# Optimization experiments

Measured on AMD Instinct MI355X. Metric: run time of the kernel, lower is better.

Reference implementation:

```python
import jax, jax.numpy as jnp
import numpy as np

D = 256; H = 8; HD = D // H; DEPTH = 4
NGRIDS = 512; TILE = 256; IN_CHANS = 1536
MAX_SEQ = (131072 // TILE) ** 2  # 262144
_SEGS = [int(v) for v in 2.0 ** np.linspace(np.log2(1024.0), np.log2(float(MAX_SEQ)), 5)]  # [1024,4096,16384,65536,262144]
_RATIOS = [1, 2, 4, 8, 16]
LN_EPS = 1e-5


def build_pos_embed(dim, gs):
    # MAE-style 2d sincos pos embed with a leading zero row for the cls token.
    def emb1d(d, pos):
        omega = 1.0 / 10000 ** (np.arange(d // 2, dtype=np.float64) / (d / 2.0))
        out = np.einsum('m,d->md', pos.reshape(-1).astype(np.float64), omega)
        return np.concatenate([np.sin(out), np.cos(out)], axis=1)
    g = np.arange(gs, dtype=np.float64)
    gw, gh = np.meshgrid(g, g)  # meshgrid(grid_w, grid_h) as in MAE
    emb = np.concatenate([emb1d(dim // 2, gw), emb1d(dim // 2, gh)], axis=1)  # (gs*gs, dim)
    return np.concatenate([np.zeros((1, dim)), emb], axis=0).astype(np.float32)


def _ln(x, w, b):
    mu = x.mean(-1, keepdims=True)
    var = ((x - mu) ** 2).mean(-1, keepdims=True)
    return (x - mu) * jax.lax.rsqrt(var + LN_EPS) * w + b


def _dilated_attn(x, wqkv, bqkv, wo, bo):
    # LongNet dilated attention: for each (segment_len w, dilation r) branch,
    # attend within segments over a per-head strided subsample (offset = head % r),
    # then combine branches weighted by softmax log-sum-exp.
    B, L, _ = x.shape
    q, k, v = jnp.split(x @ wqkv + bqkv, 3, axis=-1)
    q = q.reshape(B, L, H, HD); k = k.reshape(B, L, H, HD); v = v.reshape(B, L, H, HD)
    scale = 1.0 / np.sqrt(HD)
    outs, lses = [], []
    for w_seg, r in zip(_SEGS, _RATIOS):
        we = min(w_seg, L); we = max((we // r) * r, r)   # effective segment length
        Lp = -(-L // we) * we; pad = Lp - L; n = Lp // we; m = we // r
        idx = (jnp.arange(H) % r)[:, None] + r * jnp.arange(m)[None, :]  # (H, m) per-head strided idx
        def seg(t):
            tp = jnp.pad(t, ((0, 0), (0, pad), (0, 0), (0, 0)))
            tp = tp.reshape(B, n, we, H, HD).transpose(0, 1, 3, 2, 4)  # (B,n,H,we,HD)
            return jnp.take_along_axis(tp, idx[None, None, :, :, None], axis=3)  # (B,n,H,m,HD)
        qs, ks, vs = seg(q), seg(k), seg(v)
        valid = (jnp.arange(Lp) < L).reshape(n, we)[:, idx]  # (n,H,m) key validity (padding mask)
        s = jnp.einsum('bnhqd,bnhkd->bnhqk', qs, ks) * scale
        s = jnp.where(valid[None, :, :, None, :], s, -jnp.inf)
        mx = jnp.maximum(jnp.max(s, axis=-1, keepdims=True), -1e30)
        p = jnp.exp(s - mx)
        den = jnp.sum(p, axis=-1, keepdims=True)
        o = jnp.einsum('bnhqk,bnhkd->bnhqd', p, vs) / jnp.maximum(den, 1e-30)
        lse = mx[..., 0] + jnp.log(jnp.maximum(den[..., 0], 1e-30))  # (B,n,H,m)
        hidx = jnp.arange(H)[:, None]
        of = jnp.zeros((B, n, H, we, HD), x.dtype).at[:, :, hidx, idx].set(o)
        lf = jnp.full((B, n, H, we), -jnp.inf, x.dtype).at[:, :, hidx, idx].set(lse)
        outs.append(of.transpose(0, 1, 3, 2, 4).reshape(B, Lp, H, HD)[:, :L])
        lses.append(lf.transpose(0, 1, 3, 2).reshape(B, Lp, H)[:, :L])
    lse_all = jnp.stack(lses)                         # (S,B,L,H)
    out_all = jnp.stack(outs)                         # (S,B,L,H,HD)
    wgt = jnp.exp(lse_all - jnp.max(lse_all, axis=0, keepdims=True))
    o = jnp.sum(wgt[..., None] * out_all, axis=0) / jnp.sum(wgt, axis=0)[..., None]
    return o.reshape(B, L, D) @ wo + bo


def _forward(x, coords, patch_w, patch_b, cls_token, pos_embed, ln1_w, ln1_b, wqkv, bqkv,
             wo, bo, ln2_w, ln2_b, w1, b1, w2, b2, encln_w, encln_b, norm_w, norm_b):
    B = x.shape[0]
    h = x @ patch_w + patch_b                                   # patch embed (Linear)
    g = jnp.floor(coords / TILE)
    pos = (g[..., 0] * NGRIDS + g[..., 1]).astype(jnp.int32) + 1  # coords_to_pos
    h = h + pos_embed[pos]                                      # irregular pos-embed gather
    cls = jnp.broadcast_to(cls_token + pos_embed[0], (B, 1, D))
    h = jnp.concatenate([cls, h], axis=1)                       # (B, 4096, D)

    def step(hc, p):
        l1w, l1b, qw, qb, ow, ob, l2w, l2b, f1w, f1b, f2w, f2b = p
        hc = hc + _dilated_attn(_ln(hc, l1w, l1b), qw, qb, ow, ob)
        f = jax.nn.gelu(_ln(hc, l2w, l2b) @ f1w + f1b, approximate=False) @ f2w + f2b
        return hc + f, None

    h, _ = jax.lax.scan(step, h, (ln1_w, ln1_b, wqkv, bqkv, wo, bo, ln2_w, ln2_b, w1, b1, w2, b2))
    h = _ln(h, encln_w, encln_b)          # encoder final LN (pre-LN stack)
    return _ln(h, norm_w, norm_b)[:, 0]   # global_pool=False: normed cls token, (B, D)


def setup_inputs() -> dict:
    key = jax.random.key(0)
    ks = jax.random.split(key, 8)
    B, N = 1, 4095
    s = 0.02
    rn = lambda k, shape: jax.random.normal(k, shape, jnp.float32) * s
    return dict(
        x=jax.random.normal(ks[0], (B, N, IN_CHANS), jnp.float32),
        coords=jax.random.randint(ks[1], (B, N, 2), 0, TILE * NGRIDS).astype(jnp.float32),
        patch_w=rn(ks[2], (IN_CHANS, D)), patch_b=jnp.zeros((D,), jnp.float32),
        cls_token=rn(ks[3], (1, 1, D)),
        pos_embed=jnp.asarray(build_pos_embed(D, NGRIDS)),
        ln1_w=jnp.ones((DEPTH, D), jnp.float32), ln1_b=jnp.zeros((DEPTH, D), jnp.float32),
        wqkv=rn(ks[4], (DEPTH, D, 3 * D)), bqkv=jnp.zeros((DEPTH, 3 * D), jnp.float32),
        wo=rn(ks[5], (DEPTH, D, D)), bo=jnp.zeros((DEPTH, D), jnp.float32),
        ln2_w=jnp.ones((DEPTH, D), jnp.float32), ln2_b=jnp.zeros((DEPTH, D), jnp.float32),
        w1=rn(ks[6], (DEPTH, D, 4 * D)), b1=jnp.zeros((DEPTH, 4 * D), jnp.float32),
        w2=rn(ks[7], (DEPTH, 4 * D, D)), b2=jnp.zeros((DEPTH, D), jnp.float32),
        encln_w=jnp.ones((D,), jnp.float32), encln_b=jnp.zeros((D,), jnp.float32),
        norm_w=jnp.ones((D,), jnp.float32), norm_b=jnp.zeros((D,), jnp.float32),
    )


def reference(x, coords, patch_w, patch_b, cls_token, pos_embed, ln1_w, ln1_b, wqkv, bqkv,
              wo, bo, ln2_w, ln2_b, w1, b1, w2, b2, encln_w, encln_b, norm_w, norm_b):
    return _forward(x, coords, patch_w, patch_b, cls_token, pos_embed, ln1_w, ln1_b, wqkv, bqkv,
                    wo, bo, ln2_w, ln2_b, w1, b1, w2, b2, encln_w, encln_b, norm_w, norm_b)
```

## Files before the change

kernel.cpp:

```cpp
#include <hip/hip_runtime.h>
#include <hip/hip_bf16.h>
#include <math.h>


typedef __attribute__((ext_vector_type(8))) short short8;
typedef __attribute__((ext_vector_type(4))) float f32x4;

__device__ __forceinline__ float wred_sum(float v) {
#pragma unroll
  for (int o = 32; o; o >>= 1) v += __shfl_xor(v, o);
  return v;
}

__device__ __forceinline__ unsigned short f2bf(float x) {
  unsigned u = __float_as_uint(x);
  u += 0x7FFF + ((u >> 16) & 1);
  return (unsigned short)(u >> 16);
}
__device__ __forceinline__ float bf2f(unsigned short s) {
  return __uint_as_float(((unsigned)s) << 16);
}

__global__ __launch_bounds__(256) void prep_kernel(
    const float* __restrict__ pw, const float* __restrict__ wqkv,
    const float* __restrict__ wo, const float* __restrict__ w1,
    const float* __restrict__ w2, unsigned short* __restrict__ wt,
    const float* __restrict__ x, unsigned short* __restrict__ xb) {
  __shared__ float T[32][33];
  if (blockIdx.x >= 3456) {
    const int i = (blockIdx.x - 3456) * 256 + threadIdx.x;
    const int row = i / 192, k8 = i % 192;
    const int k = k8 * 8;
    size_t dst = ((size_t)(row >> 4) * 48 + (k >> 5)) * 512 +
                 (size_t)(row & 15) * 32 + (k & 31);
    if (row >= 4095) {
      *(uint4*)(xb + dst) = make_uint4(0, 0, 0, 0);
      return;
    }
    const float4 a = *(const float4*)(x + (size_t)row * 1536 + k);
    const float4 b = *(const float4*)(x + (size_t)row * 1536 + k + 4);
    unsigned u0 = (unsigned)f2bf(a.x) | ((unsigned)f2bf(a.y) << 16);
    unsigned u1 = (unsigned)f2bf(a.z) | ((unsigned)f2bf(a.w) << 16);
    unsigned u2 = (unsigned)f2bf(b.x) | ((unsigned)f2bf(b.y) << 16);
    unsigned u3 = (unsigned)f2bf(b.z) | ((unsigned)f2bf(b.w) << 16);
    *(uint4*)(xb + dst) = make_uint4(u0, u1, u2, u3);
    return;
  }
  const int bid = blockIdx.x;
  const float* src;
  int Kd, Nd, lt;
  size_t doff;
  if (bid < 384) {
    src = pw; Kd = 1536; Nd = 256; doff = 0; lt = bid;
  } else if (bid < 1152) {
    int l = (bid - 384) / 192, r = (bid - 384) % 192;
    src = wqkv + (size_t)l * 196608; Kd = 256; Nd = 768;
    doff = 393216 + (size_t)l * 196608; lt = r;
  } else if (bid < 1408) {
    int l = (bid - 1152) / 64, r = (bid - 1152) % 64;
    src = wo + (size_t)l * 65536; Kd = 256; Nd = 256;
    doff = 1179648 + (size_t)l * 65536; lt = r;
  } else if (bid < 2432) {
    int l = (bid - 1408) / 256, r = (bid - 1408) % 256;
    src = w1 + (size_t)l * 262144; Kd = 256; Nd = 1024;
    doff = 1441792 + (size_t)l * 262144; lt = r;
  } else {
    int l = (bid - 2432) / 256, r = (bid - 2432) % 256;
    src = w2 + (size_t)l * 262144; Kd = 1024; Nd = 256;
    doff = 2490368 + (size_t)l * 262144; lt = r;
  }
  const int tilesK = Kd >> 5;
  const int tn = lt / tilesK, tk = lt % tilesK;
  const int k0 = tk * 32, n0 = tn * 32;
  const int t = threadIdx.x;
  const int rr = t >> 3, c4 = t & 7;
  float4 v = *(const float4*)(src + (size_t)(k0 + rr) * Nd + n0 + c4 * 4);
  T[rr][c4 * 4 + 0] = v.x;
  T[rr][c4 * 4 + 1] = v.y;
  T[rr][c4 * 4 + 2] = v.z;
  T[rr][c4 * 4 + 3] = v.w;
  __syncthreads();
  float o0 = T[c4 * 4 + 0][rr], o1 = T[c4 * 4 + 1][rr];
  float o2 = T[c4 * 4 + 2][rr], o3 = T[c4 * 4 + 3][rr];
  unsigned u0 = (unsigned)f2bf(o0) | ((unsigned)f2bf(o1) << 16);
  unsigned u1 = (unsigned)f2bf(o2) | ((unsigned)f2bf(o3) << 16);
  const int n = n0 + rr;
  size_t fo = doff + ((size_t)(n >> 4) * (Kd >> 5) + (k0 >> 5)) * 512 +
              (size_t)(n & 15) * 32 + c4 * 4;
  *(uint2*)(wt + fo) = make_uint2(u0, u1);
}

__global__ __launch_bounds__(256) void gemm_patch(
    const unsigned short* __restrict__ Af, const unsigned short* __restrict__ Bt,
    const float* __restrict__ bias, const float* __restrict__ coords,
    const float* __restrict__ cls, const float* __restrict__ pe,
    float* __restrict__ h) {
  const int lane = threadIdx.x & 63, w = threadIdx.x >> 6;
  const int g = lane >> 4, q = lane & 15;
  const int bm = blockIdx.x * 64, bn = blockIdx.y * 32;

  const unsigned short* ap =
      Af + ((size_t)((bm >> 4) + w) * 48) * 512 + q * 32 + 8 * g;
  const unsigned short* bp = Bt + q * 32 + 8 * g;

  f32x4 acc[2];
#pragma unroll
  for (int i = 0; i < 2; i++) acc[i] = (f32x4){0.f, 0.f, 0.f, 0.f};

#pragma unroll 4
  for (int ks = 0; ks < 48; ks++) {
    short8 af = *(const short8*)(ap + (size_t)ks * 512);
#pragma unroll
    for (int cf = 0; cf < 2; cf++) {
      short8 bf = *(const short8*)(bp +
          ((size_t)(((bn >> 4) + cf) * 48 + ks)) * 512);
      acc[cf] = __builtin_amdgcn_mfma_f32_16x16x32_bf16(af, bf, acc[cf], 0, 0, 0);
    }
  }

  const int orow0 = bm + 16 * w + 4 * g;
  int prow[4];
#pragma unroll
  for (int rg = 0; rg < 4; rg++) {
    int orow = orow0 + rg;
    orow = orow < 4095 ? orow : 4094;
    float c0 = coords[(size_t)orow * 2 + 0];
    float c1 = coords[(size_t)orow * 2 + 1];
    prow[rg] = (int)floorf(c0 * (1.f / 256.f)) * 512 +
               (int)floorf(c1 * (1.f / 256.f)) + 1;
  }
#pragma unroll
  for (int cf = 0; cf < 2; cf++) {
    const int col = bn + 16 * cf + q;
    const float bs = bias[col];
#pragma unroll
    for (int rg = 0; rg < 4; rg++) {
      int orow = orow0 + rg;
      if (orow < 4095) {
        float c = acc[cf][rg] + bs + pe[(size_t)prow[rg] * 256 + col];
        h[(size_t)(orow + 1) * 256 + col] = c;
      }
    }
  }
  if (blockIdx.x == 0 && blockIdx.y == 0 && threadIdx.x < 64) {
    float4 cv = *(const float4*)(cls + threadIdx.x * 4);
    float4 pv = *(const float4*)(pe + threadIdx.x * 4);
    *(float4*)(h + threadIdx.x * 4) =
        make_float4(cv.x + pv.x, cv.y + pv.y, cv.z + pv.z, cv.w + pv.w);
  }
}

__global__ __launch_bounds__(256) void ln_bf16_kernel(
    const float* __restrict__ x, const float* __restrict__ wg,
    const float* __restrict__ b, unsigned short* __restrict__ y) {
  const int row = blockIdx.x * 4 + (threadIdx.x >> 6);
  const int lane = threadIdx.x & 63;
  float4 v = *(const float4*)(x + (size_t)row * 256 + lane * 4);
  float s1 = wred_sum(v.x + v.y + v.z + v.w);
  float s2 = wred_sum(v.x * v.x + v.y * v.y + v.z * v.z + v.w * v.w);
  float mu = s1 * (1.f / 256.f);
  float inv = rsqrtf(s2 * (1.f / 256.f) - mu * mu + 1e-5f);
  float4 wv = *(const float4*)(wg + lane * 4);
  float4 bv = *(const float4*)(b + lane * 4);
  float o0 = (v.x - mu) * inv * wv.x + bv.x;
  float o1 = (v.y - mu) * inv * wv.y + bv.y;
  float o2 = (v.z - mu) * inv * wv.z + bv.z;
  float o3 = (v.w - mu) * inv * wv.w + bv.w;
  unsigned u0 = (unsigned)f2bf(o0) | ((unsigned)f2bf(o1) << 16);
  unsigned u1 = (unsigned)f2bf(o2) | ((unsigned)f2bf(o3) << 16);
  size_t addr = ((size_t)(row >> 4) * 8 + (lane >> 3)) * 512 +
                (size_t)(row & 15) * 32 + (lane & 7) * 4;
  *(uint2*)(y + addr) = make_uint2(u0, u1);
}

template <int EPI>
__global__ __launch_bounds__(256) void gemm_af(
    const unsigned short* __restrict__ Af, const unsigned short* __restrict__ Bt,
    const float* __restrict__ bias, unsigned short* __restrict__ Cv, int N) {
  const int lane = threadIdx.x & 63, w = threadIdx.x >> 6;
  const int g = lane >> 4, q = lane & 15;
  const int bm = blockIdx.x * 64, bn = blockIdx.y * 64;
  const unsigned short* ap =
      Af + ((size_t)((bm >> 4) + w) * 8) * 512 + q * 32 + 8 * g;
  const unsigned short* bp = Bt + q * 32 + 8 * g;

  f32x4 acc[4];
#pragma unroll
  for (int i = 0; i < 4; i++) acc[i] = (f32x4){0.f, 0.f, 0.f, 0.f};

#pragma unroll
  for (int ks = 0; ks < 8; ks++) {
    short8 af = *(const short8*)(ap + (size_t)ks * 512);
#pragma unroll
    for (int cf = 0; cf < 4; cf++) {
      short8 bf = *(const short8*)(bp +
          ((size_t)((bn >> 4) + cf) * 8 + ks) * 512);
      acc[cf] = __builtin_amdgcn_mfma_f32_16x16x32_bf16(af, bf, acc[cf], 0, 0, 0);
    }
  }

  const int orow0 = bm + 16 * w + 4 * g;
#pragma unroll
  for (int cf = 0; cf < 4; cf++) {
    const int col = bn + 16 * cf + q;
    const float bs = bias[col];
#pragma unroll
    for (int rg = 0; rg < 4; rg++) {
      float c = acc[cf][rg] + bs;
      const int orow = orow0 + rg;
      if (EPI == 1) {
        c = 0.5f * c * (1.f + erff(c * 0.70710678118654752f));
        const int cq = 16 * cf + q;
        size_t idx = ((size_t)(orow >> 4) * (N >> 5) + (bn >> 5) + (cq >> 5)) *
                         512 +
                     (size_t)(orow & 15) * 32 + (cq & 31);
        Cv[idx] = f2bf(c);
      } else {
        Cv[(size_t)orow * N + col] = f2bf(c);
      }
    }
  }
}

__global__ __launch_bounds__(256) void gemm_proj(
    const unsigned short* __restrict__ Af, const unsigned short* __restrict__ Bt,
    const float* __restrict__ bias, float* __restrict__ C) {
  const int lane = threadIdx.x & 63, w = threadIdx.x >> 6;
  const int g = lane >> 4, q = lane & 15;
  const int bm = blockIdx.x * 64, bn = blockIdx.y * 32;
  const unsigned short* ap =
      Af + ((size_t)((bm >> 4) + w) * 8) * 512 + q * 32 + 8 * g;
  const unsigned short* bp = Bt + q * 32 + 8 * g;

  f32x4 acc[2];
#pragma unroll
  for (int i = 0; i < 2; i++) acc[i] = (f32x4){0.f, 0.f, 0.f, 0.f};

#pragma unroll
  for (int ks = 0; ks < 8; ks++) {
    short8 af = *(const short8*)(ap + (size_t)ks * 512);
#pragma unroll
    for (int cf = 0; cf < 2; cf++) {
      short8 bf = *(const short8*)(bp +
          ((size_t)((bn >> 4) + cf) * 8 + ks) * 512);
      acc[cf] = __builtin_amdgcn_mfma_f32_16x16x32_bf16(af, bf, acc[cf], 0, 0, 0);
    }
  }

  const int orow0 = bm + 16 * w + 4 * g;
#pragma unroll
  for (int cf = 0; cf < 2; cf++) {
    const int col = bn + 16 * cf + q;
    const float bs = bias[col];
#pragma unroll
    for (int rg = 0; rg < 4; rg++)
      C[(size_t)(orow0 + rg) * 256 + col] += acc[cf][rg] + bs;
  }
}

__global__ __launch_bounds__(256) void gemm_mlp2(
    const unsigned short* __restrict__ Af, const unsigned short* __restrict__ Bt,
    const float* __restrict__ bias, float* __restrict__ C) {
  const int lane = threadIdx.x & 63, w = threadIdx.x >> 6;
  const int g = lane >> 4, q = lane & 15;
  const int bm = blockIdx.x * 64, bn = blockIdx.y * 32;
  const unsigned short* ap =
      Af + ((size_t)((bm >> 4) + w) * 32) * 512 + q * 32 + 8 * g;
  const unsigned short* bp = Bt + q * 32 + 8 * g;

  f32x4 acc[2];
#pragma unroll
  for (int i = 0; i < 2; i++) acc[i] = (f32x4){0.f, 0.f, 0.f, 0.f};

#pragma unroll 4
  for (int ks = 0; ks < 32; ks++) {
    short8 af = *(const short8*)(ap + (size_t)ks * 512);
#pragma unroll
    for (int cf = 0; cf < 2; cf++) {
      short8 bf = *(const short8*)(bp +
          ((size_t)((bn >> 4) + cf) * 32 + ks) * 512);
      acc[cf] = __builtin_amdgcn_mfma_f32_16x16x32_bf16(af, bf, acc[cf], 0, 0, 0);
    }
  }

  const int orow0 = bm + 16 * w + 4 * g;
#pragma unroll
  for (int cf = 0; cf < 2; cf++) {
    const int col = bn + 16 * cf + q;
    const float bs = bias[col];
#pragma unroll
    for (int rg = 0; rg < 4; rg++)
      C[(size_t)(orow0 + rg) * 256 + col] += acc[cf][rg] + bs;
  }
}

__device__ __forceinline__ void decode_gather(int bid, int& r, int& m,
                                              int& off, int& base, int& h,
                                              int& kt, int& ub) {
  const int c = bid & 7;
  const int j = bid >> 3;
  if (j < 64) {
    int u = c + 8 * (j >> 4);
    kt = j & 15;
    r = 1; m = 1024; base = (u >> 3) * 1024; h = u & 7; off = 0; ub = u * 32768;
  } else if (j < 96) {
    int jj = j - 64;
    int grp = c + 8 * (jj >> 4);
    h = grp >> 1;
    kt = (grp & 1) * 16 + (jj & 15);
    r = 2; m = 2048; base = 0; off = h & 1; ub = 1048576 + h * 65536;
  } else if (j < 112) {
    h = c; kt = j - 96;
    r = 4; m = 1024; base = 0; off = h & 3; ub = 1572864 + h * 32768;
  } else if (j < 120) {
    h = c; kt = j - 112;
    r = 8; m = 512; base = 0; off = h & 7; ub = 1835008 + h * 16384;
  } else {
    h = c; kt = j - 120;
    r = 16; m = 256; base = 0; off = h; ub = 1966080 + h * 8192;
  }
}

__global__ __launch_bounds__(256) void gather_kernel(
    const unsigned short* __restrict__ qkvb, unsigned short* __restrict__ kg,
    unsigned short* __restrict__ vt) {
  __shared__ unsigned short T[32][64];
  int r, m, off, base, h, kt, ub;
  decode_gather(blockIdx.x, r, m, off, base, h, kt, ub);
  const int t = threadIdx.x;
  {
    int key = t >> 2, c = t & 3;
    size_t row = base + off + (size_t)r * (kt * 64 + key);
    const unsigned short* src = qkvb + row * 768 + h * 32 + 8 * c;
    short8 kk = *(const short8*)(src + 256);
    int gk = kt * 64 + key;
    *(short8*)(kg + ub + (size_t)(gk >> 4) * 512 + (size_t)(gk & 15) * 32 +
               8 * c) = kk;
    short8 vv = *(const short8*)(src + 512);
#pragma unroll
    for (int i = 0; i < 8; i++) T[8 * c + i][key] = (unsigned short)vv[i];
  }
  __syncthreads();
  int dim = t >> 3, c8 = t & 7;
  int vk = kt * 64 + 8 * c8;
  *(short8*)(vt + ub + ((size_t)(vk >> 5) * 2 + (dim >> 4)) * 512 +
             (size_t)(dim & 15) * 32 + (vk & 31)) = *(const short8*)&T[dim][8 * c8];
}

__device__ __forceinline__ void decode_attn(int bid, int& slot, int& r, int& m,
                                            int& nt, int& koff, int& off,
                                            int& base, int& h, int& qt,
                                            int& ub) {
  const int c = bid & 7;
  const int j = bid >> 3;
  if (j < 64) {
    int u = c + 8 * (j >> 4);
    qt = j & 15;
    slot = 0; r = 1; m = 1024; nt = 16; koff = 0;
    base = (u >> 3) * 1024; h = u & 7; off = 0; ub = u * 32768;
  } else if (j < 128) {
    int jj = j - 64;
    int grp = c + 8 * (jj >> 5);
    h = grp >> 1;
    int half = grp & 1;
    qt = jj & 31;
    slot = 1 + half; r = 2; m = 2048; nt = 16; koff = half * 1024;
    base = 0; off = h & 1; ub = 1048576 + h * 65536;
  } else if (j < 144) {
    h = c; qt = j - 128;
    slot = 3; r = 4; m = 1024; nt = 16; koff = 0;
    base = 0; off = h & 3; ub = 1572864 + h * 32768;
  } else if (j < 152) {
    h = c; qt = j - 144;
    slot = 4; r = 8; m = 512; nt = 8; koff = 0;
    base = 0; off = h & 7; ub = 1835008 + h * 16384;
  } else {
    h = c; qt = j - 152;
    slot = 5; r = 16; m = 256; nt = 4; koff = 0;
    base = 0; off = h; ub = 1966080 + h * 8192;
  }
}

__global__ __launch_bounds__(256) void attn_mfma_kernel(
    const unsigned short* __restrict__ qkvb,
    const unsigned short* __restrict__ kg, const unsigned short* __restrict__ vt,
    unsigned short* __restrict__ oa, float* __restrict__ lse_all) {
  int slot, r, m, nt, koff, off, base, h, qt, ub;
  decode_attn(blockIdx.x, slot, r, m, nt, koff, off, base, h, qt, ub);

  const int lane = threadIdx.x & 63;
  const int wid = threadIdx.x >> 6;
  const int g = lane >> 4, q = lane & 15;
  const int q0 = qt * 64 + wid * 16;

  const size_t qrow = base + off + (size_t)r * (q0 + q);
  short8 qf = *(const short8*)(qkvb + qrow * 768 + h * 32 + 8 * g);

  const unsigned short* kp = kg + ub + q * 32 + 8 * g;
  const unsigned short* vp = vt + ub + q * 32 + 8 * g;
  const int kt0 = koff >> 4;
  const int vt0 = koff >> 5;

  f32x4 ot0 = {0.f, 0.f, 0.f, 0.f}, ot1 = {0.f, 0.f, 0.f, 0.f};
  float rl = 0.f;
  const float scale = 0.17677669529663687f;

  short8 kf[4];
#pragma unroll
  for (int a = 0; a < 4; a++)
    kf[a] = *(const short8*)(kp + (size_t)(kt0 + a) * 512);

  for (int kt = 0; kt < nt; ++kt) {
    const int k0 = kt * 64;
    const int v2 = vt0 + (k0 >> 5);
    short8 va0 = *(const short8*)(vp + (size_t)(v2 * 2 + 0) * 512);
    short8 vb0 = *(const short8*)(vp + (size_t)(v2 * 2 + 1) * 512);
    short8 va1 = *(const short8*)(vp + (size_t)((v2 + 1) * 2 + 0) * 512);
    short8 vb1 = *(const short8*)(vp + (size_t)((v2 + 1) * 2 + 1) * 512);

    f32x4 st[4];
#pragma unroll
    for (int a = 0; a < 4; a++) {
      f32x4 z = {0.f, 0.f, 0.f, 0.f};
      st[a] = __builtin_amdgcn_mfma_f32_16x16x32_bf16(kf[a], qf, z, 0, 0, 0);
    }
    if (kt + 1 < nt) {
#pragma unroll
      for (int a = 0; a < 4; a++)
        kf[a] = *(const short8*)(kp + (size_t)(kt0 + ((k0 + 64) >> 4) + a) * 512);
    }

    float p[4][4];
    float tl = 0.f;
#pragma unroll
    for (int a = 0; a < 4; a++)
#pragma unroll
      for (int rr = 0; rr < 4; rr++) {
        p[a][rr] = __expf(st[a][rr] * scale);
        tl += p[a][rr];
      }
    tl += __shfl_xor(tl, 16);
    tl += __shfl_xor(tl, 32);
    rl += tl;

    unsigned pk[4][2];
#pragma unroll
    for (int a = 0; a < 4; a++) {
      asm("v_cvt_pk_bf16_f32 %0, %1, %2"
          : "=v"(pk[a][0]) : "v"(p[a][0]), "v"(p[a][1]));
      asm("v_cvt_pk_bf16_f32 %0, %1, %2"
          : "=v"(pk[a][1]) : "v"(p[a][2]), "v"(p[a][3]));
    }

#pragma unroll
    for (int kk = 0; kk < 2; kk++) {
      union { unsigned w[4]; short8 v; } pb;
#pragma unroll
      for (int jj = 0; jj < 2; jj++) {
        int src = q + 16 * ((2 * g + jj) & 3);
#pragma unroll
        for (int d = 0; d < 2; d++) {
          unsigned lo = (unsigned)__shfl((int)pk[2 * kk + 0][d], src);
          unsigned hi = (unsigned)__shfl((int)pk[2 * kk + 1][d], src);
          pb.w[jj * 2 + d] = (g >> 1) ? hi : lo;
        }
      }
      if (kk == 0) {
        ot0 = __builtin_amdgcn_mfma_f32_16x16x32_bf16(va0, pb.v, ot0, 0, 0, 0);
        ot1 = __builtin_amdgcn_mfma_f32_16x16x32_bf16(vb0, pb.v, ot1, 0, 0, 0);
      } else {
        ot0 = __builtin_amdgcn_mfma_f32_16x16x32_bf16(va1, pb.v, ot0, 0, 0, 0);
        ot1 = __builtin_amdgcn_mfma_f32_16x16x32_bf16(vb1, pb.v, ot1, 0, 0, 0);
      }
    }
  }

  float inv = 1.f / rl;
  int pos = base + off + r * (q0 + q);
  size_t ob = (((size_t)(slot * 256 + (pos >> 4)) * 8 + h) * 16 + (pos & 15)) * 32;
  unsigned w0 = (unsigned)f2bf(ot0[0] * inv) | ((unsigned)f2bf(ot0[1] * inv) << 16);
  unsigned w1 = (unsigned)f2bf(ot0[2] * inv) | ((unsigned)f2bf(ot0[3] * inv) << 16);
  unsigned w2 = (unsigned)f2bf(ot1[0] * inv) | ((unsigned)f2bf(ot1[1] * inv) << 16);
  unsigned w3 = (unsigned)f2bf(ot1[2] * inv) | ((unsigned)f2bf(ot1[3] * inv) << 16);
  *(uint2*)(oa + ob + 4 * g) = make_uint2(w0, w1);
  *(uint2*)(oa + ob + 16 + 4 * g) = make_uint2(w2, w3);
  if (g == 0)
    lse_all[((size_t)slot * 4096 + pos) * 8 + h] = __logf(rl);
}

__global__ __launch_bounds__(256) void combine_kernel(
    const unsigned short* __restrict__ oa, const float* __restrict__ lse_all,
    unsigned short* __restrict__ attb) {
  const int pt = blockIdx.x >> 3, ph = blockIdx.x & 7;
  const int t = threadIdx.x;
  const int d0 = (t & 15) * 2;
  const int pl = t >> 4;
  const int pos = pt * 16 + pl;

  const int msk[6] = {0, 1, 1, 3, 7, 15};
  float l[6];
  bool cov[6];
#pragma unroll
  for (int s = 0; s < 6; s++) {
    cov[s] = ((pos ^ ph) & msk[s]) == 0;
    l[s] = cov[s] ? lse_all[((size_t)s * 4096 + pos) * 8 + ph] : -3.0e38f;
  }
  float mx = l[0];
#pragma unroll
  for (int s = 1; s < 6; s++) mx = fmaxf(mx, l[s]);
  float wsum = 0.f, o0 = 0.f, o1 = 0.f;
#pragma unroll
  for (int s = 0; s < 6; s++) {
    if (cov[s]) {
      float wg = __expf(l[s] - mx);
      wsum += wg;
      unsigned u = *(const unsigned*)(oa +
          (((size_t)(s * 256 + pt) * 8 + ph) * 16 + pl) * 32 + d0);
      o0 += wg * bf2f((unsigned short)(u & 0xFFFF));
      o1 += wg * bf2f((unsigned short)(u >> 16));
    }
  }
  float inv = 1.f / wsum;
  unsigned u = (unsigned)f2bf(o0 * inv) | ((unsigned)f2bf(o1 * inv) << 16);
  *(unsigned*)(attb + ((size_t)pt * 8 + ph) * 512 + pl * 32 + d0) = u;
}

__global__ __launch_bounds__(64) void final_kernel(
    const float* __restrict__ h, const float* __restrict__ ew,
    const float* __restrict__ eb, const float* __restrict__ nw,
    const float* __restrict__ nb, float* __restrict__ out) {
  const int lane = threadIdx.x;
  float4 v = *(const float4*)(h + lane * 4);
  float s1 = wred_sum(v.x + v.y + v.z + v.w);
  float s2 = wred_sum(v.x * v.x + v.y * v.y + v.z * v.z + v.w * v.w);
  float mu = s1 * (1.f / 256.f);
  float inv = rsqrtf(s2 * (1.f / 256.f) - mu * mu + 1e-5f);
  float4 wv = *(const float4*)(ew + lane * 4);
  float4 bv = *(const float4*)(eb + lane * 4);
  float4 tv;
  tv.x = (v.x - mu) * inv * wv.x + bv.x;
  tv.y = (v.y - mu) * inv * wv.y + bv.y;
  tv.z = (v.z - mu) * inv * wv.z + bv.z;
  tv.w = (v.w - mu) * inv * wv.w + bv.w;
  s1 = wred_sum(tv.x + tv.y + tv.z + tv.w);
  s2 = wred_sum(tv.x * tv.x + tv.y * tv.y + tv.z * tv.z + tv.w * tv.w);
  mu = s1 * (1.f / 256.f);
  inv = rsqrtf(s2 * (1.f / 256.f) - mu * mu + 1e-5f);
  float4 w2v = *(const float4*)(nw + lane * 4);
  float4 b2v = *(const float4*)(nb + lane * 4);
  float4 o;
  o.x = (tv.x - mu) * inv * w2v.x + b2v.x;
  o.y = (tv.y - mu) * inv * w2v.y + b2v.y;
  o.z = (tv.z - mu) * inv * w2v.z + b2v.z;
  o.w = (tv.w - mu) * inv * w2v.w + b2v.w;
  *(float4*)(out + lane * 4) = o;
}


extern "C" void kernel_launch(void* const* d_in, const int* in_sizes, int n_in,
                              void* d_out, int out_size, void* d_ws,
                              size_t ws_size, hipStream_t stream) {
  const float* x      = (const float*)d_in[0];
  const float* coords = (const float*)d_in[1];
  const float* pw     = (const float*)d_in[2];
  const float* pb     = (const float*)d_in[3];
  const float* cls    = (const float*)d_in[4];
  const float* pe     = (const float*)d_in[5];
  const float* ln1w   = (const float*)d_in[6];
  const float* ln1b   = (const float*)d_in[7];
  const float* wqkv   = (const float*)d_in[8];
  const float* bqkv   = (const float*)d_in[9];
  const float* wo     = (const float*)d_in[10];
  const float* bo     = (const float*)d_in[11];
  const float* ln2w   = (const float*)d_in[12];
  const float* ln2b   = (const float*)d_in[13];
  const float* w1     = (const float*)d_in[14];
  const float* b1     = (const float*)d_in[15];
  const float* w2     = (const float*)d_in[16];
  const float* b2     = (const float*)d_in[17];
  const float* encw   = (const float*)d_in[18];
  const float* encb   = (const float*)d_in[19];
  const float* nw     = (const float*)d_in[20];
  const float* nb     = (const float*)d_in[21];

  float* ws = (float*)d_ws;
  float* h              = ws;
  unsigned short* hnbf  = (unsigned short*)(ws + 1048576);
  unsigned short* qkvb  = (unsigned short*)(ws + 1572864);
  unsigned short* kg    = (unsigned short*)(ws + 3145728);
  unsigned short* vt    = (unsigned short*)(ws + 4161536);
  unsigned short* oa    = (unsigned short*)(ws + 5177344);
  float* lse            = ws + 8323072;
  unsigned short* attb  = (unsigned short*)(ws + 8519680);
  unsigned short* midb  = (unsigned short*)(ws + 9043968);
  unsigned short* xb    = (unsigned short*)(ws + 11141120);
  unsigned short* wt    = (unsigned short*)(ws + 14286848);

  prep_kernel<<<6528, 256, 0, stream>>>(pw, wqkv, wo, w1, w2, wt, x, xb);
  gemm_patch<<<dim3(64, 8), 256, 0, stream>>>(xb, wt, pb, coords, cls, pe, h);

  for (int l = 0; l < 4; l++) {
    ln_bf16_kernel<<<1024, 256, 0, stream>>>(h, ln1w + l * 256, ln1b + l * 256,
                                             hnbf);
    gemm_af<3><<<dim3(64, 12), 256, 0, stream>>>(
        hnbf, wt + 393216 + (size_t)l * 196608, bqkv + l * 768, qkvb, 768);
    gather_kernel<<<992, 256, 0, stream>>>(qkvb, kg, vt);
    attn_mfma_kernel<<<1248, 256, 0, stream>>>(qkvb, kg, vt, oa, lse);
    combine_kernel<<<2048, 256, 0, stream>>>(oa, lse, attb);
    gemm_proj<<<dim3(64, 8), 256, 0, stream>>>(
        attb, wt + 1179648 + (size_t)l * 65536, bo + l * 256, h);
    ln_bf16_kernel<<<1024, 256, 0, stream>>>(h, ln2w + l * 256, ln2b + l * 256,
                                             hnbf);
    gemm_af<1><<<dim3(64, 16), 256, 0, stream>>>(
        hnbf, wt + 1441792 + (size_t)l * 262144, b1 + l * 1024, midb, 1024);
    gemm_mlp2<<<dim3(64, 8), 256, 0, stream>>>(
        midb, wt + 2490368 + (size_t)l * 262144, b2 + l * 256, h);
  }

  final_kernel<<<1, 64, 0, stream>>>(h, encw, encb, nw, nb, (float*)d_out);
}
```

Before: 435.6 us.

## Fuse LayerNorm into the A-operand load of the QKV and MLP1 GEMMs

Stores the fp32 residual stream in the MFMA fragment-tiled layout so GEMMs can read it directly. The separate LayerNorm-to-bf16 kernels are removed, and the QKV and MLP1 GEMMs now compute the row statistics themselves, normalising and converting to bf16 in registers. This drops eight launches and a bf16 round trip per forward pass. In exchange, every column-block recomputes the LayerNorm and reads the fp32 rows, which doubles A-operand traffic and uses more registers.

```diff
diff --git a/kernel.cpp b/kernel.cpp
--- a/kernel.cpp
+++ b/kernel.cpp
@@ -5,12 +5,6 @@
 
 typedef __attribute__((ext_vector_type(8))) short short8;
 typedef __attribute__((ext_vector_type(4))) float f32x4;
-
-__device__ __forceinline__ float wred_sum(float v) {
-#pragma unroll
-  for (int o = 32; o; o >>= 1) v += __shfl_xor(v, o);
-  return v;
-}
 
 __device__ __forceinline__ unsigned short f2bf(float x) {
   unsigned u = __float_as_uint(x);
@@ -94,7 +88,7 @@
     const unsigned short* __restrict__ Af, const unsigned short* __restrict__ Bt,
     const float* __restrict__ bias, const float* __restrict__ coords,
     const float* __restrict__ cls, const float* __restrict__ pe,
-    float* __restrict__ h) {
+    float* __restrict__ hf) {
   const int lane = threadIdx.x & 63, w = threadIdx.x >> 6;
   const int g = lane >> 4, q = lane & 15;
   const int bm = blockIdx.x * 64, bn = blockIdx.y * 32;
@@ -138,64 +132,80 @@
       int orow = orow0 + rg;
       if (orow < 4095) {
         float c = acc[cf][rg] + bs + pe[(size_t)prow[rg] * 256 + col];
-        h[(size_t)(orow + 1) * 256 + col] = c;
+        int row = orow + 1;
+        size_t fo = ((size_t)(row >> 4) * 8 + (col >> 5)) * 512 +
+                    (size_t)(row & 15) * 32 + (col & 31);
+        hf[fo] = c;
       }
     }
   }
   if (blockIdx.x == 0 && blockIdx.y == 0 && threadIdx.x < 64) {
     float4 cv = *(const float4*)(cls + threadIdx.x * 4);
     float4 pv = *(const float4*)(pe + threadIdx.x * 4);
-    *(float4*)(h + threadIdx.x * 4) =
+    size_t fo = (size_t)(threadIdx.x >> 3) * 512 + (threadIdx.x & 7) * 4;
+    *(float4*)(hf + fo) =
         make_float4(cv.x + pv.x, cv.y + pv.y, cv.z + pv.z, cv.w + pv.w);
   }
 }
 
-__global__ __launch_bounds__(256) void ln_bf16_kernel(
-    const float* __restrict__ x, const float* __restrict__ wg,
-    const float* __restrict__ b, unsigned short* __restrict__ y) {
-  const int row = blockIdx.x * 4 + (threadIdx.x >> 6);
-  const int lane = threadIdx.x & 63;
-  float4 v = *(const float4*)(x + (size_t)row * 256 + lane * 4);
-  float s1 = wred_sum(v.x + v.y + v.z + v.w);
-  float s2 = wred_sum(v.x * v.x + v.y * v.y + v.z * v.z + v.w * v.w);
-  float mu = s1 * (1.f / 256.f);
-  float inv = rsqrtf(s2 * (1.f / 256.f) - mu * mu + 1e-5f);
-  float4 wv = *(const float4*)(wg + lane * 4);
-  float4 bv = *(const float4*)(b + lane * 4);
-  float o0 = (v.x - mu) * inv * wv.x + bv.x;
-  float o1 = (v.y - mu) * inv * wv.y + bv.y;
-  float o2 = (v.z - mu) * inv * wv.z + bv.z;
-  float o3 = (v.w - mu) * inv * wv.w + bv.w;
-  unsigned u0 = (unsigned)f2bf(o0) | ((unsigned)f2bf(o1) << 16);
-  unsigned u1 = (unsigned)f2bf(o2) | ((unsigned)f2bf(o3) << 16);
-  size_t addr = ((size_t)(row >> 4) * 8 + (lane >> 3)) * 512 +
-                (size_t)(row & 15) * 32 + (lane & 7) * 4;
-  *(uint2*)(y + addr) = make_uint2(u0, u1);
-}
-
 template <int EPI>
-__global__ __launch_bounds__(256) void gemm_af(
-    const unsigned short* __restrict__ Af, const unsigned short* __restrict__ Bt,
+__global__ __launch_bounds__(256) void gemm_lnA(
+    const float* __restrict__ Hf, const unsigned short* __restrict__ Bt,
+    const float* __restrict__ lnw, const float* __restrict__ lnb,
     const float* __restrict__ bias, unsigned short* __restrict__ Cv, int N) {
   const int lane = threadIdx.x & 63, w = threadIdx.x >> 6;
   const int g = lane >> 4, q = lane & 15;
   const int bm = blockIdx.x * 64, bn = blockIdx.y * 64;
-  const unsigned short* ap =
-      Af + ((size_t)((bm >> 4) + w) * 8) * 512 + q * 32 + 8 * g;
+  const float* ap = Hf + ((size_t)((bm >> 4) + w) * 8) * 512 + q * 32 + 8 * g;
   const unsigned short* bp = Bt + q * 32 + 8 * g;
 
+  float a[8][8];
+  float s1 = 0.f, s2 = 0.f;
+#pragma unroll
+  for (int ks = 0; ks < 8; ks++) {
+    float4 u = *(const float4*)(ap + (size_t)ks * 512);
+    float4 v = *(const float4*)(ap + (size_t)ks * 512 + 4);
+    a[ks][0] = u.x; a[ks][1] = u.y; a[ks][2] = u.z; a[ks][3] = u.w;
+    a[ks][4] = v.x; a[ks][5] = v.y; a[ks][6] = v.z; a[ks][7] = v.w;
+#pragma unroll
+    for (int j = 0; j < 8; j++) {
+      s1 += a[ks][j];
+      s2 += a[ks][j] * a[ks][j];
+    }
+  }
+  s1 += __shfl_xor(s1, 16); s1 += __shfl_xor(s1, 32);
+  s2 += __shfl_xor(s2, 16); s2 += __shfl_xor(s2, 32);
+  const float mu = s1 * (1.f / 256.f);
+  const float inv = rsqrtf(s2 * (1.f / 256.f) - mu * mu + 1e-5f);
+
   f32x4 acc[4];
 #pragma unroll
   for (int i = 0; i < 4; i++) acc[i] = (f32x4){0.f, 0.f, 0.f, 0.f};
 
 #pragma unroll
   for (int ks = 0; ks < 8; ks++) {
-    short8 af = *(const short8*)(ap + (size_t)ks * 512);
+    float4 wv0 = *(const float4*)(lnw + 32 * ks + 8 * g);
+    float4 wv1 = *(const float4*)(lnw + 32 * ks + 8 * g + 4);
+    float4 bv0 = *(const float4*)(lnb + 32 * ks + 8 * g);
+    float4 bv1 = *(const float4*)(lnb + 32 * ks + 8 * g + 4);
+    float n0 = (a[ks][0] - mu) * inv * wv0.x + bv0.x;
+    float n1 = (a[ks][1] - mu) * inv * wv0.y + bv0.y;
+    float n2 = (a[ks][2] - mu) * inv * wv0.z + bv0.z;
+    float n3 = (a[ks][3] - mu) * inv * wv0.w + bv0.w;
+    float n4 = (a[ks][4] - mu) * inv * wv1.x + bv1.x;
+    float n5 = (a[ks][5] - mu) * inv * wv1.y + bv1.y;
+    float n6 = (a[ks][6] - mu) * inv * wv1.z + bv1.z;
+    float n7 = (a[ks][7] - mu) * inv * wv1.w + bv1.w;
+    union { unsigned u[4]; short8 v; } af;
+    af.u[0] = (unsigned)f2bf(n0) | ((unsigned)f2bf(n1) << 16);
+    af.u[1] = (unsigned)f2bf(n2) | ((unsigned)f2bf(n3) << 16);
+    af.u[2] = (unsigned)f2bf(n4) | ((unsigned)f2bf(n5) << 16);
+    af.u[3] = (unsigned)f2bf(n6) | ((unsigned)f2bf(n7) << 16);
 #pragma unroll
     for (int cf = 0; cf < 4; cf++) {
       short8 bf = *(const short8*)(bp +
           ((size_t)((bn >> 4) + cf) * 8 + ks) * 512);
-      acc[cf] = __builtin_amdgcn_mfma_f32_16x16x32_bf16(af, bf, acc[cf], 0, 0, 0);
+      acc[cf] = __builtin_amdgcn_mfma_f32_16x16x32_bf16(af.v, bf, acc[cf], 0, 0, 0);
     }
   }
 
@@ -224,7 +234,7 @@
 
 __global__ __launch_bounds__(256) void gemm_proj(
     const unsigned short* __restrict__ Af, const unsigned short* __restrict__ Bt,
-    const float* __restrict__ bias, float* __restrict__ C) {
+    const float* __restrict__ bias, float* __restrict__ hf) {
   const int lane = threadIdx.x & 63, w = threadIdx.x >> 6;
   const int g = lane >> 4, q = lane & 15;
   const int bm = blockIdx.x * 64, bn = blockIdx.y * 32;
@@ -253,14 +263,18 @@
     const int col = bn + 16 * cf + q;
     const float bs = bias[col];
 #pragma unroll
-    for (int rg = 0; rg < 4; rg++)
-      C[(size_t)(orow0 + rg) * 256 + col] += acc[cf][rg] + bs;
+    for (int rg = 0; rg < 4; rg++) {
+      int row = orow0 + rg;
+      size_t fo = ((size_t)(row >> 4) * 8 + (col >> 5)) * 512 +
+                  (size_t)(row & 15) * 32 + (col & 31);
+      hf[fo] += acc[cf][rg] + bs;
+    }
   }
 }
 
 __global__ __launch_bounds__(256) void gemm_mlp2(
     const unsigned short* __restrict__ Af, const unsigned short* __restrict__ Bt,
-    const float* __restrict__ bias, float* __restrict__ C) {
+    const float* __restrict__ bias, float* __restrict__ hf) {
   const int lane = threadIdx.x & 63, w = threadIdx.x >> 6;
   const int g = lane >> 4, q = lane & 15;
   const int bm = blockIdx.x * 64, bn = blockIdx.y * 32;
@@ -289,8 +303,12 @@
     const int col = bn + 16 * cf + q;
     const float bs = bias[col];
 #pragma unroll
-    for (int rg = 0; rg < 4; rg++)
-      C[(size_t)(orow0 + rg) * 256 + col] += acc[cf][rg] + bs;
+    for (int rg = 0; rg < 4; rg++) {
+      int row = orow0 + rg;
+      size_t fo = ((size_t)(row >> 4) * 8 + (col >> 5)) * 512 +
+                  (size_t)(row & 15) * 32 + (col & 31);
+      hf[fo] += acc[cf][rg] + bs;
+    }
   }
 }
 
@@ -526,13 +544,19 @@
 }
 
 __global__ __launch_bounds__(64) void final_kernel(
-    const float* __restrict__ h, const float* __restrict__ ew,
+    const float* __restrict__ hf, const float* __restrict__ ew,
     const float* __restrict__ eb, const float* __restrict__ nw,
     const float* __restrict__ nb, float* __restrict__ out) {
   const int lane = threadIdx.x;
-  float4 v = *(const float4*)(h + lane * 4);
-  float s1 = wred_sum(v.x + v.y + v.z + v.w);
-  float s2 = wred_sum(v.x * v.x + v.y * v.y + v.z * v.z + v.w * v.w);
+  size_t fo = (size_t)(lane >> 3) * 512 + (lane & 7) * 4;
+  float4 v = *(const float4*)(hf + fo);
+  float s1 = v.x + v.y + v.z + v.w;
+  float s2 = v.x * v.x + v.y * v.y + v.z * v.z + v.w * v.w;
+#pragma unroll
+  for (int o = 32; o; o >>= 1) {
+    s1 += __shfl_xor(s1, o);
+    s2 += __shfl_xor(s2, o);
+  }
   float mu = s1 * (1.f / 256.f);
   float inv = rsqrtf(s2 * (1.f / 256.f) - mu * mu + 1e-5f);
   float4 wv = *(const float4*)(ew + lane * 4);
@@ -542,8 +566,13 @@
   tv.y = (v.y - mu) * inv * wv.y + bv.y;
   tv.z = (v.z - mu) * inv * wv.z + bv.z;
   tv.w = (v.w - mu) * inv * wv.w + bv.w;
-  s1 = wred_sum(tv.x + tv.y + tv.z + tv.w);
-  s2 = wred_sum(tv.x * tv.x + tv.y * tv.y + tv.z * tv.z + tv.w * tv.w);
+  s1 = tv.x + tv.y + tv.z + tv.w;
+  s2 = tv.x * tv.x + tv.y * tv.y + tv.z * tv.z + tv.w * tv.w;
+#pragma unroll
+  for (int o = 32; o; o >>= 1) {
+    s1 += __shfl_xor(s1, o);
+    s2 += __shfl_xor(s2, o);
+  }
   mu = s1 * (1.f / 256.f);
   inv = rsqrtf(s2 * (1.f / 256.f) - mu * mu + 1e-5f);
   float4 w2v = *(const float4*)(nw + lane * 4);
@@ -584,38 +613,35 @@
   const float* nb     = (const float*)d_in[21];
 
   float* ws = (float*)d_ws;
-  float* h              = ws;
-  unsigned short* hnbf  = (unsigned short*)(ws + 1048576);
-  unsigned short* qkvb  = (unsigned short*)(ws + 1572864);
-  unsigned short* kg    = (unsigned short*)(ws + 3145728);
-  unsigned short* vt    = (unsigned short*)(ws + 4161536);
-  unsigned short* oa    = (unsigned short*)(ws + 5177344);
-  float* lse            = ws + 8323072;
-  unsigned short* attb  = (unsigned short*)(ws + 8519680);
-  unsigned short* midb  = (unsigned short*)(ws + 9043968);
-  unsigned short* xb    = (unsigned short*)(ws + 11141120);
-  unsigned short* wt    = (unsigned short*)(ws + 14286848);
+  float* hf             = ws;
+  unsigned short* qkvb  = (unsigned short*)(ws + 1048576);
+  unsigned short* kg    = (unsigned short*)(ws + 2621440);
+  unsigned short* vt    = (unsigned short*)(ws + 3637248);
+  unsigned short* oa    = (unsigned short*)(ws + 4653056);
+  float* lse            = ws + 7798784;
+  unsigned short* attb  = (unsigned short*)(ws + 7995392);
+  unsigned short* midb  = (unsigned short*)(ws + 8519680);
+  unsigned short* xb    = (unsigned short*)(ws + 10616832);
+  unsigned short* wt    = (unsigned short*)(ws + 13762560);
 
   prep_kernel<<<6528, 256, 0, stream>>>(pw, wqkv, wo, w1, w2, wt, x, xb);
-  gemm_patch<<<dim3(64, 8), 256, 0, stream>>>(xb, wt, pb, coords, cls, pe, h);
+  gemm_patch<<<dim3(64, 8), 256, 0, stream>>>(xb, wt, pb, coords, cls, pe, hf);
 
   for (int l = 0; l < 4; l++) {
-    ln_bf16_kernel<<<1024, 256, 0, stream>>>(h, ln1w + l * 256, ln1b + l * 256,
-                                             hnbf);
-    gemm_af<3><<<dim3(64, 12), 256, 0, stream>>>(
-        hnbf, wt + 393216 + (size_t)l * 196608, bqkv + l * 768, qkvb, 768);
+    gemm_lnA<3><<<dim3(64, 12), 256, 0, stream>>>(
+        hf, wt + 393216 + (size_t)l * 196608, ln1w + l * 256, ln1b + l * 256,
+        bqkv + l * 768, qkvb, 768);
     gather_kernel<<<992, 256, 0, stream>>>(qkvb, kg, vt);
     attn_mfma_kernel<<<1248, 256, 0, stream>>>(qkvb, kg, vt, oa, lse);
     combine_kernel<<<2048, 256, 0, stream>>>(oa, lse, attb);
     gemm_proj<<<dim3(64, 8), 256, 0, stream>>>(
-        attb, wt + 1179648 + (size_t)l * 65536, bo + l * 256, h);
-    ln_bf16_kernel<<<1024, 256, 0, stream>>>(h, ln2w + l * 256, ln2b + l * 256,
-                                             hnbf);
-    gemm_af<1><<<dim3(64, 16), 256, 0, stream>>>(
-        hnbf, wt + 1441792 + (size_t)l * 262144, b1 + l * 1024, midb, 1024);
+        attb, wt + 1179648 + (size_t)l * 65536, bo + l * 256, hf);
+    gemm_lnA<1><<<dim3(64, 16), 256, 0, stream>>>(
+        hf, wt + 1441792 + (size_t)l * 262144, ln2w + l * 256, ln2b + l * 256,
+        b1 + l * 1024, midb, 1024);
     gemm_mlp2<<<dim3(64, 8), 256, 0, stream>>>(
-        midb, wt + 2490368 + (size_t)l * 262144, b2 + l * 256, h);
-  }
-
-  final_kernel<<<1, 64, 0, stream>>>(h, encw, encb, nw, nb, (float*)d_out);
-}
+        midb, wt + 2490368 + (size_t)l * 262144, b2 + l * 256, hf);
+  }
+
+  final_kernel<<<1, 64, 0, stream>>>(hf, encw, encb, nw, nb, (float*)d_out);
+}
```

Measured after the change: 463.1 us. 1.06x slower.
